# Kernel optimization log

Hardware: AMD Instinct MI355X
Metric: run time of the kernel (lower is better)

The kernel has to match this reference:

```python
import jax, jax.numpy as jnp
import numpy as np

B, IN, OUT = 65536, 256, 256
EPS = 1e-10


def setup_inputs() -> dict:
    key = jax.random.key(0)
    k1, k2, k3 = jax.random.split(key, 3)
    x = jax.random.normal(k1, (B, IN), dtype=jnp.float32)
    # match nn.Linear default init scale roughly (kaiming-uniform-ish)
    W = jax.random.normal(k2, (OUT, IN), dtype=jnp.float32) / np.sqrt(IN)
    b = jax.random.normal(k3, (OUT,), dtype=jnp.float32) / np.sqrt(IN)
    return {"x": x, "W": W, "b": b}


def reference(x, W, b):
    # x: [B, in], W: [out, in], b: [out]
    # x_len[i] = sqrt(sum_k x[i,k]^2)  (original does x^2 @ ones^T -> same value per out col)
    x_len = jnp.sqrt(jnp.sum(x * x, axis=-1, keepdims=True))           # [B, 1]
    # w_len[j] = sqrt(sum_k W[j,k]^2)  (original does ones @ (W^2)^T -> same value per row)
    w_len = jnp.sqrt(jnp.sum(W * W, axis=-1))[None, :]                  # [1, out]
    x_len = jax.lax.stop_gradient(x_len)
    w_len = jax.lax.stop_gradient(w_len)
    b_sg = jax.lax.stop_gradient(b)
    out = x @ W.T + b                                                   # linear(x), grads flow
    out = out - b_sg[None, :]                                           # bias.data subtraction (no grad)
    out = jnp.maximum(out / (x_len * w_len), EPS)                       # cosine normalize + clamp
    out = out + b_sg[None, :]                                           # bias.data added back (no grad)
    return out
```

## Files before the change

### kernel.cpp

```cpp
#include <hip/hip_runtime.h>
#include <hip/hip_bf16.h>
#include <math.h>


using bf16x8 = __attribute__((ext_vector_type(8))) short;
using f32x4  = __attribute__((ext_vector_type(4))) float;

#define W_LDS_BYTES 131072
#define LDS_BYTES   (W_LDS_BYTES + 1024 + 1024)
#define EPS 1e-10f

__device__ __forceinline__ short f2bf(float f) {
    __bf16 h = (__bf16)f;
    return __builtin_bit_cast(short, h);
}

__global__ __launch_bounds__(512, 2) void ffn_cosnorm_kernel(
    const float* __restrict__ x, const float* __restrict__ W,
    const float* __restrict__ b, float* __restrict__ out)
{
    extern __shared__ char smem[];
    float* winv = (float*)(smem + W_LDS_BYTES);
    float* blds = (float*)(smem + W_LDS_BYTES + 1024);

    const int t    = threadIdx.x;
    const int lane = t & 63;
    const int wave = t >> 6;
    const int r16  = lane & 15;
    const int kg   = lane >> 4;
    const int rxor = (r16 & 7) << 4;
    const size_t rowb = (size_t)blockIdx.x * 256 + (size_t)wave * 32;

    const float* xp0 = x + (rowb + r16) * 256 + kg * 8;
    const float* xp1 = xp0 + 16 * 256;

    float4 f0a[8], f0b[8], f1a[8], f1b[8];
    #pragma unroll
    for (int s = 0; s < 8; ++s) {
        f0a[s] = *(const float4*)(xp0 + s * 32);
        f0b[s] = *(const float4*)(xp0 + s * 32 + 4);
        f1a[s] = *(const float4*)(xp1 + s * 32);
        f1b[s] = *(const float4*)(xp1 + s * 32 + 4);
    }

    {
        const int wrow = t >> 1;
        const int half = t & 1;
        const float* wr = W + (size_t)wrow * 256 + half * 128;
        const int rx = (wrow & 7) << 4;
        float ss = 0.f;
        #pragma unroll
        for (int i = 0; i < 16; ++i) {
            float4 a = *(const float4*)(wr + i * 8);
            float4 c = *(const float4*)(wr + i * 8 + 4);
            ss = fmaf(a.x, a.x, ss); ss = fmaf(a.y, a.y, ss);
            ss = fmaf(a.z, a.z, ss); ss = fmaf(a.w, a.w, ss);
            ss = fmaf(c.x, c.x, ss); ss = fmaf(c.y, c.y, ss);
            ss = fmaf(c.z, c.z, ss); ss = fmaf(c.w, c.w, ss);
            bf16x8 v;
            v[0] = f2bf(a.x); v[1] = f2bf(a.y); v[2] = f2bf(a.z); v[3] = f2bf(a.w);
            v[4] = f2bf(c.x); v[5] = f2bf(c.y); v[6] = f2bf(c.z); v[7] = f2bf(c.w);
            const int off = wrow * 512 + ((half * 256 + i * 16) ^ rx);
            *(bf16x8*)(smem + off) = v;
        }
        ss += __shfl_xor(ss, 1);
        if (!half) winv[wrow] = 1.0f / sqrtf(ss);
        if (t < 256) blds[t] = b[t];
    }

    bf16x8 xb0[8], xb1[8];
    float ss0 = 0.f, ss1 = 0.f;
    #pragma unroll
    for (int s = 0; s < 8; ++s) {
        float4 a = f0a[s], c = f0b[s];
        bf16x8 v;
        v[0] = f2bf(a.x); v[1] = f2bf(a.y); v[2] = f2bf(a.z); v[3] = f2bf(a.w);
        v[4] = f2bf(c.x); v[5] = f2bf(c.y); v[6] = f2bf(c.z); v[7] = f2bf(c.w);
        xb0[s] = v;
        ss0 = fmaf(a.x, a.x, ss0); ss0 = fmaf(a.y, a.y, ss0);
        ss0 = fmaf(a.z, a.z, ss0); ss0 = fmaf(a.w, a.w, ss0);
        ss0 = fmaf(c.x, c.x, ss0); ss0 = fmaf(c.y, c.y, ss0);
        ss0 = fmaf(c.z, c.z, ss0); ss0 = fmaf(c.w, c.w, ss0);
        float4 a1 = f1a[s], c1 = f1b[s];
        bf16x8 w1;
        w1[0] = f2bf(a1.x); w1[1] = f2bf(a1.y); w1[2] = f2bf(a1.z); w1[3] = f2bf(a1.w);
        w1[4] = f2bf(c1.x); w1[5] = f2bf(c1.y); w1[6] = f2bf(c1.z); w1[7] = f2bf(c1.w);
        xb1[s] = w1;
        ss1 = fmaf(a1.x, a1.x, ss1); ss1 = fmaf(a1.y, a1.y, ss1);
        ss1 = fmaf(a1.z, a1.z, ss1); ss1 = fmaf(a1.w, a1.w, ss1);
        ss1 = fmaf(c1.x, c1.x, ss1); ss1 = fmaf(c1.y, c1.y, ss1);
        ss1 = fmaf(c1.w, c1.w, ss1); ss1 = fmaf(c1.z, c1.z, ss1);
    }
    __syncthreads();

    f32x4 acc0[16], acc1[16];
    #pragma unroll
    for (int n = 0; n < 16; ++n) {
        acc0[n] = f32x4{0.f, 0.f, 0.f, 0.f};
        acc1[n] = f32x4{0.f, 0.f, 0.f, 0.f};
    }
    #pragma unroll
    for (int k0 = 0; k0 < 8; ++k0) {
        const int cswz = (k0 * 64 + kg * 16) ^ rxor;
        #pragma unroll
        for (int n = 0; n < 16; ++n) {
            const int addr = (n * 16 + r16) * 512 + cswz;
            bf16x8 wfr = *(const bf16x8*)(smem + addr);
            acc0[n] = __builtin_amdgcn_mfma_f32_16x16x32_bf16(wfr, xb0[k0], acc0[n], 0, 0, 0);
            acc1[n] = __builtin_amdgcn_mfma_f32_16x16x32_bf16(wfr, xb1[k0], acc1[n], 0, 0, 0);
        }
    }

    ss0 += __shfl_xor(ss0, 16); ss0 += __shfl_xor(ss0, 32);
    ss1 += __shfl_xor(ss1, 16); ss1 += __shfl_xor(ss1, 32);
    const float inv0 = 1.0f / sqrtf(ss0);
    const float inv1 = 1.0f / sqrtf(ss1);

    const int jb = kg * 4;
    float* op0 = out + (rowb + r16) * 256;
    float* op1 = op0 + (size_t)16 * 256;
    #pragma unroll
    for (int n = 0; n < 16; ++n) {
        float4 wv = *(const float4*)(winv + n * 16 + jb);
        float4 bv = *(const float4*)(blds + n * 16 + jb);
        f32x4 o0, o1;
        o0[0] = fmaxf(acc0[n][0] * (inv0 * wv.x), EPS) + bv.x;
        o0[1] = fmaxf(acc0[n][1] * (inv0 * wv.y), EPS) + bv.y;
        o0[2] = fmaxf(acc0[n][2] * (inv0 * wv.z), EPS) + bv.z;
        o0[3] = fmaxf(acc0[n][3] * (inv0 * wv.w), EPS) + bv.w;
        o1[0] = fmaxf(acc1[n][0] * (inv1 * wv.x), EPS) + bv.x;
        o1[1] = fmaxf(acc1[n][1] * (inv1 * wv.y), EPS) + bv.y;
        o1[2] = fmaxf(acc1[n][2] * (inv1 * wv.z), EPS) + bv.z;
        o1[3] = fmaxf(acc1[n][3] * (inv1 * wv.w), EPS) + bv.w;
        *(f32x4*)(op0 + n * 16 + jb) = o0;
        *(f32x4*)(op1 + n * 16 + jb) = o1;
    }
}

extern "C" void kernel_launch(void* const* d_in, const int* in_sizes, int n_in,
                              void* d_out, int out_size, void* d_ws, size_t ws_size,
                              hipStream_t stream) {
    const float* x = (const float*)d_in[0];
    const float* W = (const float*)d_in[1];
    const float* b = (const float*)d_in[2];
    float* out = (float*)d_out;

    hipFuncSetAttribute((const void*)ffn_cosnorm_kernel,
                        hipFuncAttributeMaxDynamicSharedMemorySize, LDS_BYTES);
    ffn_cosnorm_kernel<<<dim3(256), dim3(512), LDS_BYTES, stream>>>(x, W, b, out);
}
```

Measured before the change: 41.92 us.

## Interchange MFMA loops to finish each output column tile and store immediately

The GEMM loop is restructured so each 16-column output tile is fully accumulated over K, then normalized and stored right away, instead of accumulating all 16 tiles before any epilogue. The point is to interleave global stores with the MFMA work and to cut accumulator register pressure from 32 vector accumulators to 2. A sched_barrier after each tile stops the compiler from hoisting or merging work across tiles. In exchange, each MFMA chain is now a serial dependency of 8 steps with only two independent accumulators, which can expose MFMA latency, and the x bf16 fragments must stay live in registers throughout.

```diff
diff --git a/kernel.cpp b/kernel.cpp
--- a/kernel.cpp
+++ b/kernel.cpp
@@ -91,49 +91,43 @@
         ss1 = fmaf(c1.x, c1.x, ss1); ss1 = fmaf(c1.y, c1.y, ss1);
         ss1 = fmaf(c1.w, c1.w, ss1); ss1 = fmaf(c1.z, c1.z, ss1);
     }
-    __syncthreads();
-
-    f32x4 acc0[16], acc1[16];
-    #pragma unroll
-    for (int n = 0; n < 16; ++n) {
-        acc0[n] = f32x4{0.f, 0.f, 0.f, 0.f};
-        acc1[n] = f32x4{0.f, 0.f, 0.f, 0.f};
-    }
-    #pragma unroll
-    for (int k0 = 0; k0 < 8; ++k0) {
-        const int cswz = (k0 * 64 + kg * 16) ^ rxor;
-        #pragma unroll
-        for (int n = 0; n < 16; ++n) {
-            const int addr = (n * 16 + r16) * 512 + cswz;
-            bf16x8 wfr = *(const bf16x8*)(smem + addr);
-            acc0[n] = __builtin_amdgcn_mfma_f32_16x16x32_bf16(wfr, xb0[k0], acc0[n], 0, 0, 0);
-            acc1[n] = __builtin_amdgcn_mfma_f32_16x16x32_bf16(wfr, xb1[k0], acc1[n], 0, 0, 0);
-        }
-    }
 
     ss0 += __shfl_xor(ss0, 16); ss0 += __shfl_xor(ss0, 32);
     ss1 += __shfl_xor(ss1, 16); ss1 += __shfl_xor(ss1, 32);
     const float inv0 = 1.0f / sqrtf(ss0);
     const float inv1 = 1.0f / sqrtf(ss1);
 
+    __syncthreads();
+
     const int jb = kg * 4;
     float* op0 = out + (rowb + r16) * 256;
     float* op1 = op0 + (size_t)16 * 256;
+
     #pragma unroll
     for (int n = 0; n < 16; ++n) {
+        f32x4 acc0 = f32x4{0.f, 0.f, 0.f, 0.f};
+        f32x4 acc1 = f32x4{0.f, 0.f, 0.f, 0.f};
+        #pragma unroll
+        for (int k0 = 0; k0 < 8; ++k0) {
+            const int addr = (n * 16 + r16) * 512 + ((k0 * 64 + kg * 16) ^ rxor);
+            bf16x8 wfr = *(const bf16x8*)(smem + addr);
+            acc0 = __builtin_amdgcn_mfma_f32_16x16x32_bf16(wfr, xb0[k0], acc0, 0, 0, 0);
+            acc1 = __builtin_amdgcn_mfma_f32_16x16x32_bf16(wfr, xb1[k0], acc1, 0, 0, 0);
+        }
         float4 wv = *(const float4*)(winv + n * 16 + jb);
         float4 bv = *(const float4*)(blds + n * 16 + jb);
         f32x4 o0, o1;
-        o0[0] = fmaxf(acc0[n][0] * (inv0 * wv.x), EPS) + bv.x;
-        o0[1] = fmaxf(acc0[n][1] * (inv0 * wv.y), EPS) + bv.y;
-        o0[2] = fmaxf(acc0[n][2] * (inv0 * wv.z), EPS) + bv.z;
-        o0[3] = fmaxf(acc0[n][3] * (inv0 * wv.w), EPS) + bv.w;
-        o1[0] = fmaxf(acc1[n][0] * (inv1 * wv.x), EPS) + bv.x;
-        o1[1] = fmaxf(acc1[n][1] * (inv1 * wv.y), EPS) + bv.y;
-        o1[2] = fmaxf(acc1[n][2] * (inv1 * wv.z), EPS) + bv.z;
-        o1[3] = fmaxf(acc1[n][3] * (inv1 * wv.w), EPS) + bv.w;
+        o0[0] = fmaxf(acc0[0] * (inv0 * wv.x), EPS) + bv.x;
+        o0[1] = fmaxf(acc0[1] * (inv0 * wv.y), EPS) + bv.y;
+        o0[2] = fmaxf(acc0[2] * (inv0 * wv.z), EPS) + bv.z;
+        o0[3] = fmaxf(acc0[3] * (inv0 * wv.w), EPS) + bv.w;
+        o1[0] = fmaxf(acc1[0] * (inv1 * wv.x), EPS) + bv.x;
+        o1[1] = fmaxf(acc1[1] * (inv1 * wv.y), EPS) + bv.y;
+        o1[2] = fmaxf(acc1[2] * (inv1 * wv.z), EPS) + bv.z;
+        o1[3] = fmaxf(acc1[3] * (inv1 * wv.w), EPS) + bv.w;
         *(f32x4*)(op0 + n * 16 + jb) = o0;
         *(f32x4*)(op1 + n * 16 + jb) = o1;
+        __builtin_amdgcn_sched_barrier(0);
     }
 }
 
```

After: 36.34 us. 1.15x faster.
